# Optimization experiments

Hardware: AMD Instinct MI355X
Metric: run time of the kernel (lower is better)

## Reference

```python
import jax, jax.numpy as jnp
import numpy as np
from jax import lax

B, S, M, D, NQ = 128, 100, 50, 128, 10000


def _xavier(key, shape):
    fan_in, fan_out = shape[0], shape[-1]
    limit = float(np.sqrt(6.0 / (fan_in + fan_out)))
    return jax.random.uniform(key, shape, jnp.float32, -limit, limit)


def setup_inputs() -> dict:
    key = jax.random.key(0)
    ks = jax.random.split(key, 16)
    return {
        "question_seq": jax.random.randint(ks[0], (B, S), 0, NQ),
        "answer_seq": jax.random.randint(ks[1], (B, S), 0, 2),
        "emb": _xavier(ks[2], (NQ, D)),
        "key_matrix": _xavier(ks[3], (M, D)),
        "vu_w1": _xavier(ks[4], (2 * D, D)),
        "vu_b1": jnp.zeros((D,), jnp.float32),
        "vu_w2": _xavier(ks[5], (D, D)),
        "vu_b2": jnp.zeros((D,), jnp.float32),
        "er_w": _xavier(ks[6], (D, D)),
        "er_b": jnp.zeros((D,), jnp.float32),
        "ad_w": _xavier(ks[7], (D, D)),
        "ad_b": jnp.zeros((D,), jnp.float32),
        "out_w1": _xavier(ks[8], (2 * D, D)),
        "out_b1": jnp.zeros((D,), jnp.float32),
        "out_w2": _xavier(ks[9], (D, 1)),
        "out_b2": jnp.zeros((1,), jnp.float32),
    }


def reference(question_seq, answer_seq, emb, key_matrix,
              vu_w1, vu_b1, vu_w2, vu_b2,
              er_w, er_b, ad_w, ad_b,
              out_w1, out_b1, out_w2, out_b2):
    # q_embed for all steps: [B,S,D]; attention over memory slots: [B,S,M]
    q_emb = emb[question_seq]
    attn = jax.nn.softmax(jnp.einsum('bsd,md->bsm', q_emb, key_matrix), axis=-1)

    def step(v, inp):
        w, qe = inp                                   # w: [B,M], qe: [B,D]
        read = jnp.einsum('bm,bmd->bd', w, v)         # attention read
        u = jnp.concatenate([read, qe], axis=-1)      # [B,2D]
        h = jnp.tanh(u @ vu_w1 + vu_b1)
        up = h @ vu_w2 + vu_b2                        # update vector [B,D]
        e = jax.nn.sigmoid(up @ er_w + er_b)          # erase gate
        a = jnp.tanh(up @ ad_w + ad_b)                # add vector
        v = v * (1.0 - w[:, :, None] * e[:, None, :]) + w[:, :, None] * a[:, None, :]
        return v, None

    v0 = jnp.zeros((B, M, D), q_emb.dtype)
    vT, _ = lax.scan(step, v0, (attn.transpose(1, 0, 2), q_emb.transpose(1, 0, 2)))

    # predict with last question (target_question=None branch)
    last_qe = q_emb[:, -1]                            # [B,D]
    last_w = attn[:, -1]                              # [B,M]
    read = jnp.einsum('bm,bmd->bd', last_w, vT)
    p_in = jnp.concatenate([read, last_qe], axis=-1)
    h = jax.nn.relu(p_in @ out_w1 + out_b1)
    pred = jax.nn.sigmoid(h @ out_w2 + out_b2)[:, 0]  # [B]
    return pred
```

## Files before the change

kernel.cpp:

```cpp
#include <hip/hip_runtime.h>

#define BB 128
#define SS 100
#define MM 50
#define DD 128
#define KROW 66

typedef float f32x2 __attribute__((ext_vector_type(2)));

#if defined(__has_builtin)
#  if __has_builtin(__builtin_elementwise_fma)
#    define HAVE_PKFMA 1
#  endif
#  if __has_builtin(__builtin_amdgcn_update_dpp)
#    define HAVE_DPP 1
#  endif
#  if __has_builtin(__builtin_amdgcn_rcpf)
#    define HAVE_RCP 1
#  endif
#endif

__device__ __forceinline__ f32x2 pkfma(f32x2 a, f32x2 b, f32x2 c) {
#ifdef HAVE_PKFMA
    return __builtin_elementwise_fma(a, b, c);
#else
    f32x2 r; r.x = fmaf(a.x, b.x, c.x); r.y = fmaf(a.y, b.y, c.y); return r;
#endif
}

__device__ __forceinline__ float qbf_add(float x) {
#ifdef HAVE_DPP
    union { float f; int i; } c, o;
    c.f = x;
    o.i = __builtin_amdgcn_update_dpp(0, c.i, 0xB1, 0xF, 0xF, true);
    x += o.f;
    c.f = x;
    o.i = __builtin_amdgcn_update_dpp(0, c.i, 0x4E, 0xF, 0xF, true);
    return x + o.f;
#else
    x += __shfl_xor(x, 1);
    x += __shfl_xor(x, 2);
    return x;
#endif
}

__device__ __forceinline__ void barrier_lgkm() {
    asm volatile("s_waitcnt lgkmcnt(0)" ::: "memory");
    __builtin_amdgcn_s_barrier();
    __builtin_amdgcn_sched_barrier(0);
}

__device__ __forceinline__ float bf2f(unsigned short u) {
    union { unsigned int i; float f; } c; c.i = ((unsigned int)u) << 16; return c.f;
}
__device__ __forceinline__ float bfu_lo(unsigned int u) {
    union { unsigned int i; float f; } c; c.i = u << 16; return c.f;
}
__device__ __forceinline__ float bfu_hi(unsigned int u) {
    union { unsigned int i; float f; } c; c.i = u & 0xffff0000u; return c.f;
}
__device__ __forceinline__ unsigned short f2bf_bits(float f) {
    union { float f; unsigned int u; } c; c.f = f;
    unsigned int r = (c.u + 0x7FFFu + ((c.u >> 16) & 1u)) >> 16;
    return (unsigned short)r;
}
__device__ __forceinline__ unsigned int packbf(float lo, float hi) {
    return (unsigned int)f2bf_bits(lo) | ((unsigned int)f2bf_bits(hi) << 16);
}
__device__ __forceinline__ float fast_rcp(float x) {
#ifdef HAVE_RCP
    return __builtin_amdgcn_rcpf(x);
#else
    return 1.0f / x;
#endif
}
__device__ __forceinline__ float fast_sigmoid(float x) {
    return fast_rcp(1.0f + __expf(-x));
}
__device__ __forceinline__ float fast_tanh(float x) {
    float ax = fabsf(x);
    float z = __expf(-2.0f * ax);
    float r = (1.0f - z) * fast_rcp(1.0f + z);
    return copysignf(r, x);
}

template <bool BF16>
__device__ __forceinline__ float ldw(const void* p, size_t idx) {
    if (BF16) return bf2f(((const unsigned short*)p)[idx]);
    return ((const float*)p)[idx];
}

__device__ __forceinline__ bool detect_bf16(const void* emb) {
    const unsigned int* eu = (const unsigned int*)emb;
    int cnt = 0;
    for (int i = 0; i < 32; ++i) {
        unsigned int e8 = (eu[i] >> 7) & 0xFFu;
        cnt += (e8 >= 100u && e8 <= 127u) ? 1 : 0;
    }
    return cnt >= 16;
}

#define W2ROW(r) ((r) * 68 + (((r) >> 5) << 3))

#define WS_WROW_OFF 0u
#define WS_QP_OFF   (BB * SS * 32u * 4u)
#define WS_W2EA_OFF (WS_QP_OFF + BB * SS * DD * 2u)
#define WS_EAB_OFF  (WS_W2EA_OFF + DD * DD * 8u)
#define WS_NEED     (WS_EAB_OFF + DD * 8u)

struct __align__(16) SmemA {
    union {
        struct {
            unsigned int key_w[MM * KROW];
            unsigned int qe8[8][68];
        } pre;
        unsigned int w2s[8724];
    } u;
};

template <bool BF16>
__device__ void pre_impl(const int* qseq, const void* emb, const void* key,
                         const void* vu_w1, unsigned int* wrow_g, unsigned short* qp_g,
                         SmemA& sm)
{
    const int t = threadIdx.x;
    const int b = blockIdx.x;
    const int half = blockIdx.y;
    const int l = t & 63;
    const int wv = t >> 6;
    const int q = l & 3;
    const int d = (wv << 4) + (l >> 2);

    if (BF16) {
        const unsigned int* kg = (const unsigned int*)key;
        for (int g = t; g < MM * 64; g += 512)
            sm.u.pre.key_w[(g >> 6) * KROW + (g & 63)] = kg[g];
    } else {
        const float* kf = (const float*)key;
        for (int g = t; g < MM * 64; g += 512) {
            int row = g >> 6, c2 = g & 63;
            sm.u.pre.key_w[row * KROW + c2] = packbf(kf[row * 128 + 2 * c2], kf[row * 128 + 2 * c2 + 1]);
        }
    }

    float rw1b[32];
#pragma unroll
    for (int i = 0; i < 32; ++i)
        rw1b[i] = ldw<BF16>(vu_w1, (size_t)(DD + 32 * q + i) * DD + d);
    __syncthreads();

    for (int ii = 0; ii < 7; ++ii) {
        const int nrows = (ii == 6) ? 2 : 8;
        {
            int r = t >> 6, w = t & 63;
            if (r < nrows) {
                int s = 50 * half + 8 * ii + r;
                int row = qseq[b * SS + s];
                if (BF16) {
                    sm.u.pre.qe8[r][w] = ((const unsigned int*)emb)[((size_t)row << 6) + w];
                } else {
                    const float* ef = (const float*)emb + (((size_t)row) << 7) + 2 * w;
                    sm.u.pre.qe8[r][w] = packbf(ef[0], ef[1]);
                }
            }
        }
        __syncthreads();

        if (wv < nrows) {
            int m = l;
            int mc = (m < MM) ? m : (MM - 1);
            float a0 = 0.f, a1 = 0.f, a2 = 0.f, a3 = 0.f;
#pragma unroll
            for (int j = 0; j < 32; ++j) {
                uint2 kw = *(const uint2*)&sm.u.pre.key_w[mc * KROW + 2 * j];
                uint2 qw = *(const uint2*)&sm.u.pre.qe8[wv][2 * j];
                a0 = fmaf(bfu_lo(kw.x), bfu_lo(qw.x), a0);
                a1 = fmaf(bfu_hi(kw.x), bfu_hi(qw.x), a1);
                a2 = fmaf(bfu_lo(kw.y), bfu_lo(qw.y), a2);
                a3 = fmaf(bfu_hi(kw.y), bfu_hi(qw.y), a3);
            }
            float lg = (a0 + a1) + (a2 + a3);
            if (m >= MM) lg = -1e30f;
            float mx = lg;
#pragma unroll
            for (int o = 32; o > 0; o >>= 1) mx = fmaxf(mx, __shfl_xor(mx, o));
            float p = (m < MM) ? __expf(lg - mx) : 0.f;
            float sum = p;
#pragma unroll
            for (int o = 32; o > 0; o >>= 1) sum += __shfl_xor(sum, o);
            p = p * fast_rcp(sum);
            float pn = __shfl_xor(p, 4);
            int s = 50 * half + 8 * ii + wv;
            if ((m & 4) == 0)
                wrow_g[(size_t)(b * SS + s) * 32 + (m & 3) * 8 + (m >> 3)] = packbf(p, pn);
        }

        for (int sr = 0; sr < nrows; ++sr) {
            float p0 = 0.f, p1 = 0.f;
#pragma unroll
            for (int i = 0; i < 16; ++i) {
                unsigned int uw = sm.u.pre.qe8[sr][16 * q + i];
                p0 = fmaf(rw1b[2 * i],     bfu_lo(uw), p0);
                p1 = fmaf(rw1b[2 * i + 1], bfu_hi(uw), p1);
            }
            float qpv = qbf_add(p0 + p1);
            int s = 50 * half + 8 * ii + sr;
            if (q == 0) qp_g[(size_t)(b * SS + s) * DD + d] = f2bf_bits(qpv);
        }
        __syncthreads();
    }
}

template <bool BF16>
__device__ void build_impl(const void* vu_w2, const void* vu_b2,
                           const void* er_w, const void* er_b,
                           const void* ad_w, const void* ad_b,
                           f32x2* w2ea_g, f32x2* eab_g, SmemA& sm)
{
    const int t = threadIdx.x;
    const int l = t & 63;
    const int wv = t >> 6;
    const int q = l & 3;
    const int d = (wv << 4) + (l >> 2);

    if (BF16) {
        const unsigned int* wg = (const unsigned int*)vu_w2;
        for (int g = t; g < 128 * 64; g += 512)
            sm.u.w2s[W2ROW(g >> 6) + (g & 63)] = wg[g];
    } else {
        const float* wf = (const float*)vu_w2;
        for (int g = t; g < 128 * 64; g += 512) {
            int row = g >> 6, c2 = g & 63;
            sm.u.w2s[W2ROW(row) + c2] = packbf(wf[row * 128 + 2 * c2], wf[row * 128 + 2 * c2 + 1]);
        }
    }
    __syncthreads();

    f32x2 rw2ea[32];
#pragma unroll
    for (int k = 0; k < 32; ++k) { rw2ea[k].x = 0.f; rw2ea[k].y = 0.f; }
    f32x2 eab2; eab2.x = 0.f; eab2.y = 0.f;
#pragma unroll 1
    for (int jc = 0; jc < 4; ++jc) {
        f32x2 ea[32];
#pragma unroll
        for (int i = 0; i < 32; ++i) {
            int j = 32 * jc + i;
            ea[i].x = ldw<BF16>(er_w, (size_t)j * DD + d);
            ea[i].y = ldw<BF16>(ad_w, (size_t)j * DD + d);
            float b2j = ldw<BF16>(vu_b2, j);
            f32x2 bs; bs.x = b2j; bs.y = b2j;
            eab2 = pkfma(bs, ea[i], eab2);
        }
#pragma unroll
        for (int k = 0; k < 32; ++k) {
            const uint4* wp = (const uint4*)&sm.u.w2s[W2ROW(32 * q + k) + 16 * jc];
            uint4 A = wp[0], B = wp[1], C = wp[2], Dv = wp[3];
            unsigned int W[16] = { A.x, A.y, A.z, A.w, B.x, B.y, B.z, B.w,
                                   C.x, C.y, C.z, C.w, Dv.x, Dv.y, Dv.z, Dv.w };
            f32x2 acc = rw2ea[k];
#pragma unroll
            for (int wd = 0; wd < 16; ++wd) {
                float wlo = bfu_lo(W[wd]), whi = bfu_hi(W[wd]);
                f32x2 s0; s0.x = wlo; s0.y = wlo;
                f32x2 s1; s1.x = whi; s1.y = whi;
                acc = pkfma(s0, ea[2 * wd], acc);
                acc = pkfma(s1, ea[2 * wd + 1], acc);
            }
            rw2ea[k] = acc;
        }
    }
    eab2.x += ldw<BF16>(er_b, d);
    eab2.y += ldw<BF16>(ad_b, d);

#pragma unroll
    for (int k = 0; k < 32; ++k)
        w2ea_g[(size_t)(32 * q + k) * DD + d] = rw2ea[k];
    if (q == 0) eab_g[d] = eab2;
}

__global__ __launch_bounds__(512) void DKVMN_78546361909953_pre(
    const int* __restrict__ qseq,
    const void* emb, const void* key, const void* vu_w1,
    const void* vu_w2, const void* vu_b2,
    const void* er_w, const void* er_b, const void* ad_w, const void* ad_b,
    void* ws)
{
    __shared__ SmemA sm;
    unsigned int*   wrow_g = (unsigned int*)((char*)ws + WS_WROW_OFF);
    unsigned short* qp_g   = (unsigned short*)((char*)ws + WS_QP_OFF);
    f32x2*          w2ea_g = (f32x2*)((char*)ws + WS_W2EA_OFF);
    f32x2*          eab_g  = (f32x2*)((char*)ws + WS_EAB_OFF);
    bool isbf = detect_bf16(emb);
    if (blockIdx.x < BB) {
        if (isbf) pre_impl<true>(qseq, emb, key, vu_w1, wrow_g, qp_g, sm);
        else      pre_impl<false>(qseq, emb, key, vu_w1, wrow_g, qp_g, sm);
    } else if (blockIdx.y == 0) {
        if (isbf) build_impl<true>(vu_w2, vu_b2, er_w, er_b, ad_w, ad_b, w2ea_g, eab_g, sm);
        else      build_impl<false>(vu_w2, vu_b2, er_w, er_b, ad_w, ad_b, w2ea_g, eab_g, sm);
    }
}

struct __align__(16) SmemB {
    float xread[152];
    float xh[152];
    float h1f[DD];
    float qlast[DD];
    unsigned int   wtab[SS][32];
    unsigned short qptab[SS][DD];
};

template <bool BF16>
__device__ void scan_impl(
    const int* __restrict__ qseq,
    const void* emb, const void* vu_w1, const void* vu_b1,
    const void* out_w1, const void* out_b1, const void* out_w2, const void* out_b2,
    const unsigned int* wrow_g, const unsigned short* qp_g,
    const f32x2* w2ea_g, const f32x2* eab_g,
    void* outp, SmemB& sm)
{
    const int t = threadIdx.x;
    const int b = blockIdx.x;
    const int l = t & 63;
    const int q = l & 3;
    const int d = ((t >> 6) << 4) + (l >> 2);

    {
        const uint4* srcw = (const uint4*)(wrow_g + (size_t)b * SS * 32);
        uint4* dstw = (uint4*)&sm.wtab[0][0];
        for (int g = t; g < SS * 32 / 4; g += 512) dstw[g] = srcw[g];
        const uint4* srcq = (const uint4*)(qp_g + (size_t)b * SS * DD);
        uint4* dstq = (uint4*)&sm.qptab[0][0];
        for (int g = t; g < SS * DD / 8; g += 512) dstq[g] = srcq[g];
    }

    if (t < 64) {
        int row = qseq[b * SS + (SS - 1)];
        if (BF16) {
            unsigned int uw = ((const unsigned int*)emb)[((size_t)row << 6) + t];
            sm.qlast[2 * t]     = bfu_lo(uw);
            sm.qlast[2 * t + 1] = bfu_hi(uw);
        } else {
            const float* ef = (const float*)emb + (((size_t)row) << 7) + 2 * t;
            sm.qlast[2 * t]     = ef[0];
            sm.qlast[2 * t + 1] = ef[1];
        }
    }

    f32x2 rw1a2[16];
#pragma unroll
    for (int i = 0; i < 16; ++i) {
        int k0 = 32 * q + 2 * i;
        rw1a2[i].x = ldw<BF16>(vu_w1, (size_t)k0 * DD + d);
        rw1a2[i].y = ldw<BF16>(vu_w1, (size_t)(k0 + 1) * DD + d);
    }
    const float b1r = ldw<BF16>(vu_b1, d);

    f32x2 rwe2[16], rwa2[16];
#pragma unroll
    for (int i = 0; i < 16; ++i) {
        f32x2 w0 = w2ea_g[(size_t)(32 * q + 2 * i) * DD + d];
        f32x2 w1 = w2ea_g[(size_t)(32 * q + 2 * i + 1) * DD + d];
        rwe2[i].x = w0.x; rwe2[i].y = w1.x;
        rwa2[i].x = w0.y; rwa2[i].y = w1.y;
    }
    const f32x2 eab2 = eab_g[d];

    f32x2 v2[7];
#pragma unroll
    for (int p = 0; p < 7; ++p) { v2[p].x = 0.f; v2[p].y = 0.f; }

    if (t < 152) sm.xread[t] = 0.f;
    __syncthreads();

    f32x2 wr2[7];
    {
        uint4 w0 = *(const uint4*)&sm.wtab[0][q * 8];
        uint4 w1 = *(const uint4*)&sm.wtab[0][q * 8 + 4];
        unsigned int ww[8] = { w0.x, w0.y, w0.z, w0.w, w1.x, w1.y, w1.z, w1.w };
#pragma unroll
        for (int p = 0; p < 7; ++p) { wr2[p].x = bfu_lo(ww[p]); wr2[p].y = bfu_hi(ww[p]); }
    }
    unsigned short qpcur = sm.qptab[0][d];

    for (int s = 0; s < SS; ++s) {
        uint4 pwA, pwB;
        unsigned short pq = 0;
        const bool hasnext = (s + 1 < SS);
        if (hasnext) {
            pwA = *(const uint4*)&sm.wtab[s + 1][q * 8];
            pwB = *(const uint4*)&sm.wtab[s + 1][q * 8 + 4];
            pq  = sm.qptab[s + 1][d];
        }

        {
            float hb = bf2f(qpcur) + b1r;
            const float4* xp = (const float4*)&sm.xread[40 * q];
            f32x2 acc0, acc1, acc2, acc3;
            acc0.x = 0.f; acc0.y = 0.f; acc1.x = 0.f; acc1.y = 0.f;
            acc2.x = 0.f; acc2.y = 0.f; acc3.x = 0.f; acc3.y = 0.f;
#pragma unroll
            for (int j = 0; j < 4; ++j) {
                float4 X = xp[2 * j];
                float4 Y = xp[2 * j + 1];
                f32x2 x01; x01.x = X.x; x01.y = X.y;
                f32x2 x23; x23.x = X.z; x23.y = X.w;
                f32x2 y01; y01.x = Y.x; y01.y = Y.y;
                f32x2 y23; y23.x = Y.z; y23.y = Y.w;
                acc0 = pkfma(rw1a2[4 * j],     x01, acc0);
                acc1 = pkfma(rw1a2[4 * j + 1], x23, acc1);
                acc2 = pkfma(rw1a2[4 * j + 2], y01, acc2);
                acc3 = pkfma(rw1a2[4 * j + 3], y23, acc3);
            }
            f32x2 ap = (acc0 + acc1) + (acc2 + acc3);
            float acc = qbf_add(ap.x + ap.y);
            float hh = fast_tanh(acc + hb);
            if (q == 0) sm.xh[d + 8 * (d >> 5)] = hh;
        }
        barrier_lgkm();

        {
            const float4* xp = (const float4*)&sm.xh[40 * q];
            f32x2 ae0, ae1, ae2, ae3, aa0, aa1, aa2, aa3;
            ae0.x = 0.f; ae0.y = 0.f; ae1.x = 0.f; ae1.y = 0.f;
            ae2.x = 0.f; ae2.y = 0.f; ae3.x = 0.f; ae3.y = 0.f;
            aa0.x = 0.f; aa0.y = 0.f; aa1.x = 0.f; aa1.y = 0.f;
            aa2.x = 0.f; aa2.y = 0.f; aa3.x = 0.f; aa3.y = 0.f;
#pragma unroll
            for (int j = 0; j < 4; ++j) {
                float4 X = xp[2 * j];
                float4 Y = xp[2 * j + 1];
                f32x2 h01; h01.x = X.x; h01.y = X.y;
                f32x2 h23; h23.x = X.z; h23.y = X.w;
                f32x2 h45; h45.x = Y.x; h45.y = Y.y;
                f32x2 h67; h67.x = Y.z; h67.y = Y.w;
                ae0 = pkfma(rwe2[4 * j],     h01, ae0);
                aa0 = pkfma(rwa2[4 * j],     h01, aa0);
                ae1 = pkfma(rwe2[4 * j + 1], h23, ae1);
                aa1 = pkfma(rwa2[4 * j + 1], h23, aa1);
                ae2 = pkfma(rwe2[4 * j + 2], h45, ae2);
                aa2 = pkfma(rwa2[4 * j + 2], h45, aa2);
                ae3 = pkfma(rwe2[4 * j + 3], h67, ae3);
                aa3 = pkfma(rwa2[4 * j + 3], h67, aa3);
            }
            f32x2 aep = (ae0 + ae1) + (ae2 + ae3);
            f32x2 aap = (aa0 + aa1) + (aa2 + aa3);
            float ae = qbf_add(aep.x + aep.y);
            float aa = qbf_add(aap.x + aap.y);
            float e = fast_sigmoid(ae + eab2.x);
            float a = fast_tanh(aa + eab2.y);
            f32x2 me; me.x = -e; me.y = -e;
            f32x2 av; av.x = a;  av.y = a;
#pragma unroll
            for (int p = 0; p < 7; ++p)
                v2[p] = pkfma(wr2[p], pkfma(me, v2[p], av), v2[p]);
            if (hasnext) {
                unsigned int ww[8] = { pwA.x, pwA.y, pwA.z, pwA.w, pwB.x, pwB.y, pwB.z, pwB.w };
#pragma unroll
                for (int p = 0; p < 7; ++p) { wr2[p].x = bfu_lo(ww[p]); wr2[p].y = bfu_hi(ww[p]); }
                qpcur = pq;
            }
            f32x2 rA; rA.x = 0.f; rA.y = 0.f;
            f32x2 rB; rB.x = 0.f; rB.y = 0.f;
            rA = pkfma(wr2[0], v2[0], rA); rB = pkfma(wr2[1], v2[1], rB);
            rA = pkfma(wr2[2], v2[2], rA); rB = pkfma(wr2[3], v2[3], rB);
            rA = pkfma(wr2[4], v2[4], rA); rB = pkfma(wr2[5], v2[5], rB);
            rA = pkfma(wr2[6], v2[6], rA);
            float rr = qbf_add((rA.x + rB.x) + (rA.y + rB.y));
            if (q == 0) sm.xread[rr == rr ? (d + 8 * (d >> 5)) : 0] = rr;
        }
        barrier_lgkm();
    }

    float acc = 0.f;
    {
        const float4* xp = (const float4*)&sm.xread[40 * q];
        const float4* qp4 = (const float4*)&sm.qlast[32 * q];
#pragma unroll
        for (int j = 0; j < 8; ++j) {
            float4 xv = xp[j];
            float4 qv = qp4[j];
            int k = 32 * q + 4 * j;
            acc = fmaf(ldw<BF16>(out_w1, (size_t)k * DD + d),       xv.x, acc);
            acc = fmaf(ldw<BF16>(out_w1, (size_t)(k + 1) * DD + d), xv.y, acc);
            acc = fmaf(ldw<BF16>(out_w1, (size_t)(k + 2) * DD + d), xv.z, acc);
            acc = fmaf(ldw<BF16>(out_w1, (size_t)(k + 3) * DD + d), xv.w, acc);
            acc = fmaf(ldw<BF16>(out_w1, (size_t)(DD + k) * DD + d),     qv.x, acc);
            acc = fmaf(ldw<BF16>(out_w1, (size_t)(DD + k + 1) * DD + d), qv.y, acc);
            acc = fmaf(ldw<BF16>(out_w1, (size_t)(DD + k + 2) * DD + d), qv.z, acc);
            acc = fmaf(ldw<BF16>(out_w1, (size_t)(DD + k + 3) * DD + d), qv.w, acc);
        }
    }
    acc = qbf_add(acc);
    float h1 = fmaxf(acc + ldw<BF16>(out_b1, d), 0.f);
    if (q == 0) sm.h1f[d] = h1;
    __syncthreads();

    if (t < 64) {
        float xs = fmaf(sm.h1f[t], ldw<BF16>(out_w2, t),
                        sm.h1f[64 + t] * ldw<BF16>(out_w2, 64 + t));
#pragma unroll
        for (int o = 32; o > 0; o >>= 1) xs += __shfl_xor(xs, o);
        if (t == 0) {
            float pred = fast_sigmoid(xs + ldw<BF16>(out_b2, 0));
            if (BF16) ((unsigned short*)outp)[b] = f2bf_bits(pred);
            else      ((float*)outp)[b] = pred;
        }
    }
}

__global__ __launch_bounds__(512) void DKVMN_78546361909953_scan(
    const int* __restrict__ qseq,
    const void* emb, const void* vu_w1, const void* vu_b1,
    const void* out_w1, const void* out_b1, const void* out_w2, const void* out_b2,
    void* ws, void* outp)
{
    __shared__ SmemB sm;
    const unsigned int*   wrow_g = (const unsigned int*)((char*)ws + WS_WROW_OFF);
    const unsigned short* qp_g   = (const unsigned short*)((char*)ws + WS_QP_OFF);
    const f32x2*          w2ea_g = (const f32x2*)((char*)ws + WS_W2EA_OFF);
    const f32x2*          eab_g  = (const f32x2*)((char*)ws + WS_EAB_OFF);
    if (detect_bf16(emb))
        scan_impl<true>(qseq, emb, vu_w1, vu_b1, out_w1, out_b1, out_w2, out_b2,
                        wrow_g, qp_g, w2ea_g, eab_g, outp, sm);
    else
        scan_impl<false>(qseq, emb, vu_w1, vu_b1, out_w1, out_b1, out_w2, out_b2,
                         wrow_g, qp_g, w2ea_g, eab_g, outp, sm);
}

struct __align__(16) SmemM {
    union {
        struct {
            unsigned int key_w[MM * KROW];
            unsigned int qe8[8][68];
        } pre;
        struct {
            float xread[152];
            float xhdup[312];
            float h1f[DD];
        } run;
    } u;
    union {
        unsigned int w2s[8724];
        struct {
            unsigned int wrow_p[SS][32];
            unsigned short qp_all[SS][DD];
        } tab;
    } v2;
    int qrow[SS];
    float qlast[DD];
};

template <bool BF16>
__device__ void mono_impl(
    const int* __restrict__ qseq,
    const void* emb, const void* key,
    const void* vu_w1, const void* vu_b1, const void* vu_w2, const void* vu_b2,
    const void* er_w, const void* er_b, const void* ad_w, const void* ad_b,
    const void* out_w1, const void* out_b1, const void* out_w2, const void* out_b2,
    void* outp, SmemM& sm)
{
    const int t = threadIdx.x;
    const int b = blockIdx.x;
    const int l = t & 63;
    const int wv = t >> 6;
    const int q = l & 3;
    const int d = (wv << 4) + (l >> 2);

    if (BF16) {
        const unsigned int* kg = (const unsigned int*)key;
        for (int g = t; g < MM * 64; g += 512)
            sm.u.pre.key_w[(g >> 6) * KROW + (g & 63)] = kg[g];
        const unsigned int* wg = (const unsigned int*)vu_w2;
        for (int g = t; g < 128 * 64; g += 512)
            sm.v2.w2s[W2ROW(g >> 6) + (g & 63)] = wg[g];
    } else {
        const float* kf = (const float*)key;
        for (int g = t; g < MM * 64; g += 512) {
            int row = g >> 6, c2 = g & 63;
            sm.u.pre.key_w[row * KROW + c2] = packbf(kf[row * 128 + 2 * c2], kf[row * 128 + 2 * c2 + 1]);
        }
        const float* wf = (const float*)vu_w2;
        for (int g = t; g < 128 * 64; g += 512) {
            int row = g >> 6, c2 = g & 63;
            sm.v2.w2s[W2ROW(row) + c2] = packbf(wf[row * 128 + 2 * c2], wf[row * 128 + 2 * c2 + 1]);
        }
    }
    for (int g = t; g < SS; g += 512) sm.qrow[g] = qseq[b * SS + g];
    __syncthreads();

    f32x2 rw2ea[32];
#pragma unroll
    for (int k = 0; k < 32; ++k) { rw2ea[k].x = 0.f; rw2ea[k].y = 0.f; }
    f32x2 eab2; eab2.x = 0.f; eab2.y = 0.f;
#pragma unroll 1
    for (int jc = 0; jc < 4; ++jc) {
        f32x2 ea[32];
#pragma unroll
        for (int i = 0; i < 32; ++i) {
            int j = 32 * jc + i;
            ea[i].x = ldw<BF16>(er_w, (size_t)j * DD + d);
            ea[i].y = ldw<BF16>(ad_w, (size_t)j * DD + d);
            float b2j = ldw<BF16>(vu_b2, j);
            f32x2 bs; bs.x = b2j; bs.y = b2j;
            eab2 = pkfma(bs, ea[i], eab2);
        }
#pragma unroll
        for (int k = 0; k < 32; ++k) {
            const uint4* wp = (const uint4*)&sm.v2.w2s[W2ROW(32 * q + k) + 16 * jc];
            uint4 A = wp[0], B = wp[1], C = wp[2], Dv = wp[3];
            unsigned int W[16] = { A.x, A.y, A.z, A.w, B.x, B.y, B.z, B.w,
                                   C.x, C.y, C.z, C.w, Dv.x, Dv.y, Dv.z, Dv.w };
            f32x2 acc = rw2ea[k];
#pragma unroll
            for (int wd = 0; wd < 16; ++wd) {
                float wlo = bfu_lo(W[wd]), whi = bfu_hi(W[wd]);
                f32x2 s0; s0.x = wlo; s0.y = wlo;
                f32x2 s1; s1.x = whi; s1.y = whi;
                acc = pkfma(s0, ea[2 * wd], acc);
                acc = pkfma(s1, ea[2 * wd + 1], acc);
            }
            rw2ea[k] = acc;
        }
    }
    eab2.x += ldw<BF16>(er_b, d);
    eab2.y += ldw<BF16>(ad_b, d);
    __syncthreads();

    float rw1a[32], rw1b[32];
#pragma unroll
    for (int i = 0; i < 32; ++i) {
        rw1a[i] = ldw<BF16>(vu_w1, (size_t)(32 * q + i) * DD + d);
        rw1b[i] = ldw<BF16>(vu_w1, (size_t)(DD + 32 * q + i) * DD + d);
    }
    const float b1r = ldw<BF16>(vu_b1, d);

    for (int ii = 0; ii < 13; ++ii) {
        const int nrows = (ii == 12) ? 4 : 8;
        {
            int r = t >> 6, w = t & 63;
            if (r < nrows) {
                int row = sm.qrow[8 * ii + r];
                if (BF16) {
                    sm.u.pre.qe8[r][w] = ((const unsigned int*)emb)[((size_t)row << 6) + w];
                } else {
                    const float* ef = (const float*)emb + (((size_t)row) << 7) + 2 * w;
                    sm.u.pre.qe8[r][w] = packbf(ef[0], ef[1]);
                }
            }
        }
        __syncthreads();

        if (wv < nrows) {
            int m = l;
            int mc = (m < MM) ? m : (MM - 1);
            float a0 = 0.f, a1 = 0.f, a2 = 0.f, a3 = 0.f;
#pragma unroll
            for (int j = 0; j < 32; ++j) {
                uint2 kw = *(const uint2*)&sm.u.pre.key_w[mc * KROW + 2 * j];
                uint2 qw = *(const uint2*)&sm.u.pre.qe8[wv][2 * j];
                a0 = fmaf(bfu_lo(kw.x), bfu_lo(qw.x), a0);
                a1 = fmaf(bfu_hi(kw.x), bfu_hi(qw.x), a1);
                a2 = fmaf(bfu_lo(kw.y), bfu_lo(qw.y), a2);
                a3 = fmaf(bfu_hi(kw.y), bfu_hi(qw.y), a3);
            }
            float lg = (a0 + a1) + (a2 + a3);
            if (m >= MM) lg = -1e30f;
            float mx = lg;
#pragma unroll
            for (int o = 32; o > 0; o >>= 1) mx = fmaxf(mx, __shfl_xor(mx, o));
            float p = (m < MM) ? __expf(lg - mx) : 0.f;
            float sum = p;
#pragma unroll
            for (int o = 32; o > 0; o >>= 1) sum += __shfl_xor(sum, o);
            p = p * fast_rcp(sum);
            float pn = __shfl_xor(p, 4);
            if ((m & 4) == 0)
                sm.v2.tab.wrow_p[8 * ii + wv][(m & 3) * 8 + (m >> 3)] = packbf(p, pn);
        }

        for (int sr = 0; sr < nrows; ++sr) {
            float p0 = 0.f, p1 = 0.f;
#pragma unroll
            for (int i = 0; i < 16; ++i) {
                unsigned int uw = sm.u.pre.qe8[sr][16 * q + i];
                p0 = fmaf(rw1b[2 * i],     bfu_lo(uw), p0);
                p1 = fmaf(rw1b[2 * i + 1], bfu_hi(uw), p1);
            }
            float qpv = qbf_add(p0 + p1);
            if (q == 0) sm.v2.tab.qp_all[8 * ii + sr][d] = f2bf_bits(qpv);
        }
        __syncthreads();
    }

    if (t < 64) {
        unsigned int uw = sm.u.pre.qe8[3][t];
        sm.qlast[2 * t]     = bfu_lo(uw);
        sm.qlast[2 * t + 1] = bfu_hi(uw);
    }
    f32x2 v2[7];
#pragma unroll
    for (int p = 0; p < 7; ++p) { v2[p].x = 0.f; v2[p].y = 0.f; }
    f32x2 wr2[7];
    {
        const uint4* wp = (const uint4*)&sm.v2.tab.wrow_p[0][q * 8];
        uint4 w0 = wp[0], w1 = wp[1];
        unsigned int ww[8] = { w0.x, w0.y, w0.z, w0.w, w1.x, w1.y, w1.z, w1.w };
#pragma unroll
        for (int p = 0; p < 7; ++p) { wr2[p].x = bfu_lo(ww[p]); wr2[p].y = bfu_hi(ww[p]); }
    }
    if (t < 152) sm.u.run.xread[t] = 0.f;
    __syncthreads();

    for (int s = 0; s < SS; ++s) {
        {
            float qpv = bf2f(sm.v2.tab.qp_all[s][d]);
            const float4* xp = (const float4*)&sm.u.run.xread[40 * q];
            f32x2 rw1a2_j;
            f32x2 acc2; acc2.x = 0.f; acc2.y = 0.f;
#pragma unroll
            for (int j = 0; j < 8; ++j) {
                float4 X = xp[j];
                f32x2 x01; x01.x = X.x; x01.y = X.y;
                f32x2 x23; x23.x = X.z; x23.y = X.w;
                rw1a2_j.x = rw1a[4 * j];     rw1a2_j.y = rw1a[4 * j + 1];
                acc2 = pkfma(rw1a2_j, x01, acc2);
                rw1a2_j.x = rw1a[4 * j + 2]; rw1a2_j.y = rw1a[4 * j + 3];
                acc2 = pkfma(rw1a2_j, x23, acc2);
            }
            float acc = qbf_add(acc2.x + acc2.y);
            float hh = fast_tanh(acc + qpv + b1r);
            if (q == 0) {
                f32x2 hd; hd.x = hh; hd.y = hh;
                *(f32x2*)&sm.u.run.xhdup[2 * d + 8 * ((2 * d) >> 5)] = hd;
            }
        }
        __syncthreads();

        {
            f32x2 acc2; acc2.x = 0.f; acc2.y = 0.f;
#pragma unroll
            for (int blk = 0; blk < 2; ++blk) {
                const float4* xp = (const float4*)&sm.u.run.xhdup[80 * q + 40 * blk];
#pragma unroll
                for (int j = 0; j < 8; ++j) {
                    float4 X = xp[j];
                    f32x2 s0; s0.x = X.x; s0.y = X.y;
                    f32x2 s1; s1.x = X.z; s1.y = X.w;
                    int k = 16 * blk + 2 * j;
                    acc2 = pkfma(rw2ea[k], s0, acc2);
                    acc2 = pkfma(rw2ea[k + 1], s1, acc2);
                }
            }
            float ae = qbf_add(acc2.x);
            float aa = qbf_add(acc2.y);
            float e = fast_sigmoid(ae + eab2.x);
            float a = fast_tanh(aa + eab2.y);
            f32x2 me; me.x = -e; me.y = -e;
            f32x2 av; av.x = a;  av.y = a;
#pragma unroll
            for (int p = 0; p < 7; ++p)
                v2[p] = pkfma(wr2[p], pkfma(me, v2[p], av), v2[p]);
            if (s + 1 < SS) {
                const uint4* wp = (const uint4*)&sm.v2.tab.wrow_p[s + 1][q * 8];
                uint4 w0 = wp[0], w1 = wp[1];
                unsigned int ww[8] = { w0.x, w0.y, w0.z, w0.w, w1.x, w1.y, w1.z, w1.w };
#pragma unroll
                for (int p = 0; p < 7; ++p) { wr2[p].x = bfu_lo(ww[p]); wr2[p].y = bfu_hi(ww[p]); }
            }
            f32x2 racc; racc.x = 0.f; racc.y = 0.f;
#pragma unroll
            for (int p = 0; p < 7; ++p)
                racc = pkfma(wr2[p], v2[p], racc);
            float rr = qbf_add(racc.x + racc.y);
            if (q == 0) sm.u.run.xread[d + 8 * (d >> 5)] = rr;
        }
        __syncthreads();
    }

    float acc = 0.f;
    {
        const float4* xp = (const float4*)&sm.u.run.xread[40 * q];
        const float4* qp4 = (const float4*)&sm.qlast[32 * q];
#pragma unroll
        for (int j = 0; j < 8; ++j) {
            float4 xv = xp[j];
            float4 qv = qp4[j];
            int k = 32 * q + 4 * j;
            acc = fmaf(ldw<BF16>(out_w1, (size_t)k * DD + d),       xv.x, acc);
            acc = fmaf(ldw<BF16>(out_w1, (size_t)(k + 1) * DD + d), xv.y, acc);
            acc = fmaf(ldw<BF16>(out_w1, (size_t)(k + 2) * DD + d), xv.z, acc);
            acc = fmaf(ldw<BF16>(out_w1, (size_t)(k + 3) * DD + d), xv.w, acc);
            acc = fmaf(ldw<BF16>(out_w1, (size_t)(DD + k) * DD + d),     qv.x, acc);
            acc = fmaf(ldw<BF16>(out_w1, (size_t)(DD + k + 1) * DD + d), qv.y, acc);
            acc = fmaf(ldw<BF16>(out_w1, (size_t)(DD + k + 2) * DD + d), qv.z, acc);
            acc = fmaf(ldw<BF16>(out_w1, (size_t)(DD + k + 3) * DD + d), qv.w, acc);
        }
    }
    acc = qbf_add(acc);
    float h1 = fmaxf(acc + ldw<BF16>(out_b1, d), 0.f);
    if (q == 0) sm.u.run.h1f[d] = h1;
    __syncthreads();

    if (t < 64) {
        float xs = fmaf(sm.u.run.h1f[t], ldw<BF16>(out_w2, t),
                        sm.u.run.h1f[64 + t] * ldw<BF16>(out_w2, 64 + t));
#pragma unroll
        for (int o = 32; o > 0; o >>= 1) xs += __shfl_xor(xs, o);
        if (t == 0) {
            float pred = fast_sigmoid(xs + ldw<BF16>(out_b2, 0));
            if (BF16) ((unsigned short*)outp)[b] = f2bf_bits(pred);
            else      ((float*)outp)[b] = pred;
        }
    }
}

__global__ __launch_bounds__(512) void DKVMN_78546361909953_kernel(
    const int* __restrict__ qseq,
    const void* emb, const void* key,
    const void* vu_w1, const void* vu_b1, const void* vu_w2, const void* vu_b2,
    const void* er_w, const void* er_b, const void* ad_w, const void* ad_b,
    const void* out_w1, const void* out_b1, const void* out_w2, const void* out_b2,
    void* outp)
{
    __shared__ SmemM sm;
    if (detect_bf16(emb))
        mono_impl<true>(qseq, emb, key, vu_w1, vu_b1, vu_w2, vu_b2,
                        er_w, er_b, ad_w, ad_b, out_w1, out_b1, out_w2, out_b2, outp, sm);
    else
        mono_impl<false>(qseq, emb, key, vu_w1, vu_b1, vu_w2, vu_b2,
                         er_w, er_b, ad_w, ad_b, out_w1, out_b1, out_w2, out_b2, outp, sm);
}

extern "C" void kernel_launch(void* const* d_in, const int* in_sizes, int n_in,
                              void* d_out, int out_size, void* d_ws, size_t ws_size,
                              hipStream_t stream) {
    const int* qseq = (const int*)d_in[0];
    if (ws_size >= (size_t)WS_NEED) {
        DKVMN_78546361909953_pre<<<dim3(BB + 1, 2), 512, 0, stream>>>(
            qseq, d_in[2], d_in[3], d_in[4],
            d_in[6], d_in[7], d_in[8], d_in[9], d_in[10], d_in[11], d_ws);
        DKVMN_78546361909953_scan<<<BB, 512, 0, stream>>>(
            qseq, d_in[2], d_in[4], d_in[5],
            d_in[12], d_in[13], d_in[14], d_in[15], d_ws, d_out);
    } else {
        DKVMN_78546361909953_kernel<<<BB, 512, 0, stream>>>(
            qseq, d_in[2], d_in[3], d_in[4], d_in[5], d_in[6], d_in[7],
            d_in[8], d_in[9], d_in[10], d_in[11],
            d_in[12], d_in[13], d_in[14], d_in[15], d_out);
    }
}
```

Baseline: 247.0 us.

## Use bf16 dot2 instructions and bf16 shared vectors in scan recurrence

Rewrites the per-step scan to store the read and hidden vectors in shared memory as bf16 and compute the matvecs with v_dot2_f32_bf16 on packed bf16 weight registers. Memory weights are pre-expanded to fp32 in shared memory, the loop is unrolled by two with ping-pong weight registers, exp is replaced by exp2 intrinsics, and launch bounds request two blocks per CU. The aim is to shorten the serial per-step critical path and cut register pressure, at the cost of extra bf16 rounding on intermediate activations and weights.

```diff
diff --git a/kernel.cpp b/kernel.cpp
--- a/kernel.cpp
+++ b/kernel.cpp
@@ -18,6 +18,15 @@
 #  if __has_builtin(__builtin_amdgcn_rcpf)
 #    define HAVE_RCP 1
 #  endif
+#  if __has_builtin(__builtin_amdgcn_exp2f)
+#    define EXP2(x) __builtin_amdgcn_exp2f(x)
+#  endif
+#  if __has_builtin(__builtin_amdgcn_fdot2_f32_bf16)
+#    define HAVE_DOT2BF 1
+#  endif
+#endif
+#ifndef EXP2
+#  define EXP2(x) exp2f(x)
 #endif
 
 __device__ __forceinline__ f32x2 pkfma(f32x2 a, f32x2 b, f32x2 c) {
@@ -67,6 +76,13 @@
 __device__ __forceinline__ unsigned int packbf(float lo, float hi) {
     return (unsigned int)f2bf_bits(lo) | ((unsigned int)f2bf_bits(hi) << 16);
 }
+__device__ __forceinline__ unsigned short f2bf_hw(float f) {
+#ifdef HAVE_DOT2BF
+    union { __bf16 b; unsigned short u; } c; c.b = (__bf16)f; return c.u;
+#else
+    return f2bf_bits(f);
+#endif
+}
 __device__ __forceinline__ float fast_rcp(float x) {
 #ifdef HAVE_RCP
     return __builtin_amdgcn_rcpf(x);
@@ -75,14 +91,24 @@
 #endif
 }
 __device__ __forceinline__ float fast_sigmoid(float x) {
-    return fast_rcp(1.0f + __expf(-x));
+    return fast_rcp(1.0f + EXP2(x * -1.4426950408889634f));
 }
 __device__ __forceinline__ float fast_tanh(float x) {
     float ax = fabsf(x);
-    float z = __expf(-2.0f * ax);
+    float z = EXP2(ax * -2.8853900817779268f);
     float r = (1.0f - z) * fast_rcp(1.0f + z);
     return copysignf(r, x);
 }
+
+#ifdef HAVE_DOT2BF
+typedef __bf16 bf2v __attribute__((ext_vector_type(2)));
+__device__ __forceinline__ bf2v u2bf(unsigned int u) {
+    union { unsigned int x; bf2v v; } c; c.x = u; return c.v;
+}
+__device__ __forceinline__ float dot2bf(unsigned int a, unsigned int b, float c) {
+    return __builtin_amdgcn_fdot2_f32_bf16(u2bf(a), u2bf(b), c, false);
+}
+#endif
 
 template <bool BF16>
 __device__ __forceinline__ float ldw(const void* p, size_t idx) {
@@ -302,13 +328,141 @@
 }
 
 struct __align__(16) SmemB {
-    float xread[152];
-    float xh[152];
+    unsigned short xread[144];
+    unsigned short xh[144];
     float h1f[DD];
     float qlast[DD];
-    unsigned int   wtab[SS][32];
+    f32x2 wtabf[SS][32];
     unsigned short qptab[SS][DD];
 };
+
+#ifdef HAVE_DOT2BF
+#define SCAN_E(HB)                                                          \
+    {                                                                       \
+        const uint4* xp_ = (const uint4*)&sm.xread[32 * q];                 \
+        uint4 X0 = xp_[0], X1 = xp_[1], X2 = xp_[2], X3 = xp_[3];           \
+        float a0_ = dot2bf(rw1p[0],  X0.x, (HB) * 0.25f);                   \
+        float a1_ = dot2bf(rw1p[1],  X0.y, 0.f);                            \
+        float a2_ = dot2bf(rw1p[2],  X0.z, 0.f);                            \
+        float a3_ = dot2bf(rw1p[3],  X0.w, 0.f);                            \
+        a0_ = dot2bf(rw1p[4],  X1.x, a0_);                                  \
+        a1_ = dot2bf(rw1p[5],  X1.y, a1_);                                  \
+        a2_ = dot2bf(rw1p[6],  X1.z, a2_);                                  \
+        a3_ = dot2bf(rw1p[7],  X1.w, a3_);                                  \
+        a0_ = dot2bf(rw1p[8],  X2.x, a0_);                                  \
+        a1_ = dot2bf(rw1p[9],  X2.y, a1_);                                  \
+        a2_ = dot2bf(rw1p[10], X2.z, a2_);                                  \
+        a3_ = dot2bf(rw1p[11], X2.w, a3_);                                  \
+        a0_ = dot2bf(rw1p[12], X3.x, a0_);                                  \
+        a1_ = dot2bf(rw1p[13], X3.y, a1_);                                  \
+        a2_ = dot2bf(rw1p[14], X3.z, a2_);                                  \
+        a3_ = dot2bf(rw1p[15], X3.w, a3_);                                  \
+        float u_ = qbf_add((a0_ + a1_) + (a2_ + a3_));                      \
+        float hh_ = fast_tanh(u_);                                          \
+        if (q == 0) sm.xh[d] = f2bf_hw(hh_);                                \
+    }
+#define SCAN_G_ACC                                                          \
+        const uint4* hp_ = (const uint4*)&sm.xh[32 * q];                    \
+        uint4 H0 = hp_[0], H1 = hp_[1], H2 = hp_[2], H3 = hp_[3];           \
+        float e0_ = dot2bf(rwep[0],  H0.x, eab2.x * 0.25f);                 \
+        float g0_ = dot2bf(rwap[0],  H0.x, eab2.y * 0.25f);                 \
+        float e1_ = dot2bf(rwep[1],  H0.y, 0.f);                            \
+        float g1_ = dot2bf(rwap[1],  H0.y, 0.f);                            \
+        float e2_ = dot2bf(rwep[2],  H0.z, 0.f);                            \
+        float g2_ = dot2bf(rwap[2],  H0.z, 0.f);                            \
+        float e3_ = dot2bf(rwep[3],  H0.w, 0.f);                            \
+        float g3_ = dot2bf(rwap[3],  H0.w, 0.f);                            \
+        e0_ = dot2bf(rwep[4],  H1.x, e0_);  g0_ = dot2bf(rwap[4],  H1.x, g0_); \
+        e1_ = dot2bf(rwep[5],  H1.y, e1_);  g1_ = dot2bf(rwap[5],  H1.y, g1_); \
+        e2_ = dot2bf(rwep[6],  H1.z, e2_);  g2_ = dot2bf(rwap[6],  H1.z, g2_); \
+        e3_ = dot2bf(rwep[7],  H1.w, e3_);  g3_ = dot2bf(rwap[7],  H1.w, g3_); \
+        e0_ = dot2bf(rwep[8],  H2.x, e0_);  g0_ = dot2bf(rwap[8],  H2.x, g0_); \
+        e1_ = dot2bf(rwep[9],  H2.y, e1_);  g1_ = dot2bf(rwap[9],  H2.y, g1_); \
+        e2_ = dot2bf(rwep[10], H2.z, e2_);  g2_ = dot2bf(rwap[10], H2.z, g2_); \
+        e3_ = dot2bf(rwep[11], H2.w, e3_);  g3_ = dot2bf(rwap[11], H2.w, g3_); \
+        e0_ = dot2bf(rwep[12], H3.x, e0_);  g0_ = dot2bf(rwap[12], H3.x, g0_); \
+        e1_ = dot2bf(rwep[13], H3.y, e1_);  g1_ = dot2bf(rwap[13], H3.y, g1_); \
+        e2_ = dot2bf(rwep[14], H3.z, e2_);  g2_ = dot2bf(rwap[14], H3.z, g2_); \
+        e3_ = dot2bf(rwep[15], H3.w, e3_);  g3_ = dot2bf(rwap[15], H3.w, g3_); \
+        float ae_ = qbf_add((e0_ + e1_) + (e2_ + e3_));                     \
+        float aa_ = qbf_add((g0_ + g1_) + (g2_ + g3_));
+#else
+#define SCAN_E(HB)                                                          \
+    {                                                                       \
+        const uint4* xp_ = (const uint4*)&sm.xread[32 * q];                 \
+        uint4 X0 = xp_[0], X1 = xp_[1], X2 = xp_[2], X3 = xp_[3];           \
+        unsigned int XW_[16] = { X0.x, X0.y, X0.z, X0.w, X1.x, X1.y, X1.z, X1.w, \
+                                 X2.x, X2.y, X2.z, X2.w, X3.x, X3.y, X3.z, X3.w }; \
+        float a0_ = (HB) * 0.25f, a1_ = 0.f, a2_ = 0.f, a3_ = 0.f;          \
+        _Pragma("unroll")                                                   \
+        for (int i_ = 0; i_ < 4; ++i_) {                                    \
+            a0_ = fmaf(rw1a[8 * i_ + 0], bfu_lo(XW_[4 * i_ + 0]), a0_);     \
+            a0_ = fmaf(rw1a[8 * i_ + 1], bfu_hi(XW_[4 * i_ + 0]), a0_);     \
+            a1_ = fmaf(rw1a[8 * i_ + 2], bfu_lo(XW_[4 * i_ + 1]), a1_);     \
+            a1_ = fmaf(rw1a[8 * i_ + 3], bfu_hi(XW_[4 * i_ + 1]), a1_);     \
+            a2_ = fmaf(rw1a[8 * i_ + 4], bfu_lo(XW_[4 * i_ + 2]), a2_);     \
+            a2_ = fmaf(rw1a[8 * i_ + 5], bfu_hi(XW_[4 * i_ + 2]), a2_);     \
+            a3_ = fmaf(rw1a[8 * i_ + 6], bfu_lo(XW_[4 * i_ + 3]), a3_);     \
+            a3_ = fmaf(rw1a[8 * i_ + 7], bfu_hi(XW_[4 * i_ + 3]), a3_);     \
+        }                                                                   \
+        float u_ = qbf_add((a0_ + a1_) + (a2_ + a3_));                      \
+        float hh_ = fast_tanh(u_);                                          \
+        if (q == 0) sm.xh[d] = f2bf_hw(hh_);                                \
+    }
+#define SCAN_G_ACC                                                          \
+        const uint4* hp_ = (const uint4*)&sm.xh[32 * q];                    \
+        uint4 H0 = hp_[0], H1 = hp_[1], H2 = hp_[2], H3 = hp_[3];           \
+        unsigned int HW_[16] = { H0.x, H0.y, H0.z, H0.w, H1.x, H1.y, H1.z, H1.w, \
+                                 H2.x, H2.y, H2.z, H2.w, H3.x, H3.y, H3.z, H3.w }; \
+        float ae_ = eab2.x * 0.25f, aa_ = eab2.y * 0.25f;                   \
+        float e1_ = 0.f, g1_ = 0.f;                                         \
+        _Pragma("unroll")                                                   \
+        for (int i_ = 0; i_ < 16; ++i_) {                                   \
+            float lo_ = bfu_lo(HW_[i_]), hi_ = bfu_hi(HW_[i_]);             \
+            ae_ = fmaf(rwe[2 * i_], lo_, ae_);                              \
+            e1_ = fmaf(rwe[2 * i_ + 1], hi_, e1_);                          \
+            aa_ = fmaf(rwa[2 * i_], lo_, aa_);                              \
+            g1_ = fmaf(rwa[2 * i_ + 1], hi_, g1_);                          \
+        }                                                                   \
+        ae_ = qbf_add(ae_ + e1_);                                           \
+        aa_ = qbf_add(aa_ + g1_);
+#endif
+
+#define SCAN_STEP(S, WR, WN, LAST)                                          \
+    {                                                                       \
+        float hb_ = bf2f(qpcur) + b1r;                                      \
+        if (!(LAST)) {                                                      \
+            const float4* wp4_ = (const float4*)&sm.wtabf[(S) + 1][q * 8];  \
+            float4 Aw = wp4_[0], Bw = wp4_[1], Cw = wp4_[2], Dw = wp4_[3];  \
+            WN[0] = Aw.x;  WN[1] = Aw.y;  WN[2] = Aw.z;  WN[3] = Aw.w;      \
+            WN[4] = Bw.x;  WN[5] = Bw.y;  WN[6] = Bw.z;  WN[7] = Bw.w;      \
+            WN[8] = Cw.x;  WN[9] = Cw.y;  WN[10] = Cw.z; WN[11] = Cw.w;     \
+            WN[12] = Dw.x; WN[13] = Dw.y;                                   \
+            pq = sm.qptab[(S) + 1][d];                                      \
+        }                                                                   \
+        SCAN_E(hb_)                                                         \
+        barrier_lgkm();                                                     \
+        {                                                                   \
+            SCAN_G_ACC                                                      \
+            float e_ = fast_sigmoid(ae_);                                   \
+            float a_ = fast_tanh(aa_);                                      \
+            _Pragma("unroll")                                               \
+            for (int m_ = 0; m_ < 14; ++m_)                                 \
+                vv[m_] = fmaf(WR[m_], fmaf(-e_, vv[m_], a_), vv[m_]);       \
+            const float* wu_ = (LAST) ? WR : WN;                            \
+            float r0_ = wu_[0] * vv[0], r1_ = wu_[1] * vv[1];               \
+            float r2_ = wu_[2] * vv[2], r3_ = wu_[3] * vv[3];               \
+            r0_ = fmaf(wu_[4],  vv[4],  r0_); r1_ = fmaf(wu_[5],  vv[5],  r1_); \
+            r2_ = fmaf(wu_[6],  vv[6],  r2_); r3_ = fmaf(wu_[7],  vv[7],  r3_); \
+            r0_ = fmaf(wu_[8],  vv[8],  r0_); r1_ = fmaf(wu_[9],  vv[9],  r1_); \
+            r2_ = fmaf(wu_[10], vv[10], r2_); r3_ = fmaf(wu_[11], vv[11], r3_); \
+            r0_ = fmaf(wu_[12], vv[12], r0_); r1_ = fmaf(wu_[13], vv[13], r1_); \
+            float rr_ = qbf_add((r0_ + r1_) + (r2_ + r3_));                 \
+            if (q == 0) sm.xread[d] = f2bf_hw(rr_);                         \
+            if (!(LAST)) qpcur = pq;                                        \
+        }                                                                   \
+        barrier_lgkm();                                                     \
+    }
 
 template <bool BF16>
 __device__ void scan_impl(
@@ -326,9 +480,13 @@
     const int d = ((t >> 6) << 4) + (l >> 2);
 
     {
-        const uint4* srcw = (const uint4*)(wrow_g + (size_t)b * SS * 32);
-        uint4* dstw = (uint4*)&sm.wtab[0][0];
-        for (int g = t; g < SS * 32 / 4; g += 512) dstw[g] = srcw[g];
+        const unsigned int* srcw = wrow_g + (size_t)b * SS * 32;
+        f32x2* dstw = (f32x2*)&sm.wtabf[0][0];
+        for (int g = t; g < SS * 32; g += 512) {
+            unsigned int u = srcw[g];
+            f32x2 v; v.x = bfu_lo(u); v.y = bfu_hi(u);
+            dstw[g] = v;
+        }
         const uint4* srcq = (const uint4*)(qp_g + (size_t)b * SS * DD);
         uint4* dstq = (uint4*)&sm.qptab[0][0];
         for (int g = t; g < SS * DD / 8; g += 512) dstq[g] = srcq[g];
@@ -347,144 +505,74 @@
         }
     }
 
-    f32x2 rw1a2[16];
+    const float b1r = ldw<BF16>(vu_b1, d);
+    const f32x2 eab2 = eab_g[d];
+
+#ifdef HAVE_DOT2BF
+    unsigned int rw1p[16], rwep[16], rwap[16];
 #pragma unroll
     for (int i = 0; i < 16; ++i) {
         int k0 = 32 * q + 2 * i;
-        rw1a2[i].x = ldw<BF16>(vu_w1, (size_t)k0 * DD + d);
-        rw1a2[i].y = ldw<BF16>(vu_w1, (size_t)(k0 + 1) * DD + d);
-    }
-    const float b1r = ldw<BF16>(vu_b1, d);
-
-    f32x2 rwe2[16], rwa2[16];
-#pragma unroll
-    for (int i = 0; i < 16; ++i) {
-        f32x2 w0 = w2ea_g[(size_t)(32 * q + 2 * i) * DD + d];
-        f32x2 w1 = w2ea_g[(size_t)(32 * q + 2 * i + 1) * DD + d];
-        rwe2[i].x = w0.x; rwe2[i].y = w1.x;
-        rwa2[i].x = w0.y; rwa2[i].y = w1.y;
-    }
-    const f32x2 eab2 = eab_g[d];
-
-    f32x2 v2[7];
-#pragma unroll
-    for (int p = 0; p < 7; ++p) { v2[p].x = 0.f; v2[p].y = 0.f; }
-
-    if (t < 152) sm.xread[t] = 0.f;
+        rw1p[i] = packbf(ldw<BF16>(vu_w1, (size_t)k0 * DD + d),
+                         ldw<BF16>(vu_w1, (size_t)(k0 + 1) * DD + d));
+        f32x2 w0v = w2ea_g[(size_t)k0 * DD + d];
+        f32x2 w1v = w2ea_g[(size_t)(k0 + 1) * DD + d];
+        rwep[i] = packbf(w0v.x, w1v.x);
+        rwap[i] = packbf(w0v.y, w1v.y);
+    }
+#else
+    float rw1a[32], rwe[32], rwa[32];
+#pragma unroll
+    for (int i = 0; i < 32; ++i) {
+        rw1a[i] = ldw<BF16>(vu_w1, (size_t)(32 * q + i) * DD + d);
+        f32x2 wv = w2ea_g[(size_t)(32 * q + i) * DD + d];
+        rwe[i] = wv.x; rwa[i] = wv.y;
+    }
+#endif
+
+    float vv[14];
+#pragma unroll
+    for (int m = 0; m < 14; ++m) vv[m] = 0.f;
+
+    if (t < 144) sm.xread[t] = 0;
     __syncthreads();
 
-    f32x2 wr2[7];
+    float w0[14], w1[14];
     {
-        uint4 w0 = *(const uint4*)&sm.wtab[0][q * 8];
-        uint4 w1 = *(const uint4*)&sm.wtab[0][q * 8 + 4];
-        unsigned int ww[8] = { w0.x, w0.y, w0.z, w0.w, w1.x, w1.y, w1.z, w1.w };
-#pragma unroll
-        for (int p = 0; p < 7; ++p) { wr2[p].x = bfu_lo(ww[p]); wr2[p].y = bfu_hi(ww[p]); }
+        const float4* wp4 = (const float4*)&sm.wtabf[0][q * 8];
+        float4 Aw = wp4[0], Bw = wp4[1], Cw = wp4[2], Dw = wp4[3];
+        w0[0] = Aw.x;  w0[1] = Aw.y;  w0[2] = Aw.z;  w0[3] = Aw.w;
+        w0[4] = Bw.x;  w0[5] = Bw.y;  w0[6] = Bw.z;  w0[7] = Bw.w;
+        w0[8] = Cw.x;  w0[9] = Cw.y;  w0[10] = Cw.z; w0[11] = Cw.w;
+        w0[12] = Dw.x; w0[13] = Dw.y;
     }
     unsigned short qpcur = sm.qptab[0][d];
-
-    for (int s = 0; s < SS; ++s) {
-        uint4 pwA, pwB;
-        unsigned short pq = 0;
-        const bool hasnext = (s + 1 < SS);
-        if (hasnext) {
-            pwA = *(const uint4*)&sm.wtab[s + 1][q * 8];
-            pwB = *(const uint4*)&sm.wtab[s + 1][q * 8 + 4];
-            pq  = sm.qptab[s + 1][d];
-        }
-
-        {
-            float hb = bf2f(qpcur) + b1r;
-            const float4* xp = (const float4*)&sm.xread[40 * q];
-            f32x2 acc0, acc1, acc2, acc3;
-            acc0.x = 0.f; acc0.y = 0.f; acc1.x = 0.f; acc1.y = 0.f;
-            acc2.x = 0.f; acc2.y = 0.f; acc3.x = 0.f; acc3.y = 0.f;
-#pragma unroll
-            for (int j = 0; j < 4; ++j) {
-                float4 X = xp[2 * j];
-                float4 Y = xp[2 * j + 1];
-                f32x2 x01; x01.x = X.x; x01.y = X.y;
-                f32x2 x23; x23.x = X.z; x23.y = X.w;
-                f32x2 y01; y01.x = Y.x; y01.y = Y.y;
-                f32x2 y23; y23.x = Y.z; y23.y = Y.w;
-                acc0 = pkfma(rw1a2[4 * j],     x01, acc0);
-                acc1 = pkfma(rw1a2[4 * j + 1], x23, acc1);
-                acc2 = pkfma(rw1a2[4 * j + 2], y01, acc2);
-                acc3 = pkfma(rw1a2[4 * j + 3], y23, acc3);
-            }
-            f32x2 ap = (acc0 + acc1) + (acc2 + acc3);
-            float acc = qbf_add(ap.x + ap.y);
-            float hh = fast_tanh(acc + hb);
-            if (q == 0) sm.xh[d + 8 * (d >> 5)] = hh;
-        }
-        barrier_lgkm();
-
-        {
-            const float4* xp = (const float4*)&sm.xh[40 * q];
-            f32x2 ae0, ae1, ae2, ae3, aa0, aa1, aa2, aa3;
-            ae0.x = 0.f; ae0.y = 0.f; ae1.x = 0.f; ae1.y = 0.f;
-            ae2.x = 0.f; ae2.y = 0.f; ae3.x = 0.f; ae3.y = 0.f;
-            aa0.x = 0.f; aa0.y = 0.f; aa1.x = 0.f; aa1.y = 0.f;
-            aa2.x = 0.f; aa2.y = 0.f; aa3.x = 0.f; aa3.y = 0.f;
-#pragma unroll
-            for (int j = 0; j < 4; ++j) {
-                float4 X = xp[2 * j];
-                float4 Y = xp[2 * j + 1];
-                f32x2 h01; h01.x = X.x; h01.y = X.y;
-                f32x2 h23; h23.x = X.z; h23.y = X.w;
-                f32x2 h45; h45.x = Y.x; h45.y = Y.y;
-                f32x2 h67; h67.x = Y.z; h67.y = Y.w;
-                ae0 = pkfma(rwe2[4 * j],     h01, ae0);
-                aa0 = pkfma(rwa2[4 * j],     h01, aa0);
-                ae1 = pkfma(rwe2[4 * j + 1], h23, ae1);
-                aa1 = pkfma(rwa2[4 * j + 1], h23, aa1);
-                ae2 = pkfma(rwe2[4 * j + 2], h45, ae2);
-                aa2 = pkfma(rwa2[4 * j + 2], h45, aa2);
-                ae3 = pkfma(rwe2[4 * j + 3], h67, ae3);
-                aa3 = pkfma(rwa2[4 * j + 3], h67, aa3);
-            }
-            f32x2 aep = (ae0 + ae1) + (ae2 + ae3);
-            f32x2 aap = (aa0 + aa1) + (aa2 + aa3);
-            float ae = qbf_add(aep.x + aep.y);
-            float aa = qbf_add(aap.x + aap.y);
-            float e = fast_sigmoid(ae + eab2.x);
-            float a = fast_tanh(aa + eab2.y);
-            f32x2 me; me.x = -e; me.y = -e;
-            f32x2 av; av.x = a;  av.y = a;
-#pragma unroll
-            for (int p = 0; p < 7; ++p)
-                v2[p] = pkfma(wr2[p], pkfma(me, v2[p], av), v2[p]);
-            if (hasnext) {
-                unsigned int ww[8] = { pwA.x, pwA.y, pwA.z, pwA.w, pwB.x, pwB.y, pwB.z, pwB.w };
-#pragma unroll
-                for (int p = 0; p < 7; ++p) { wr2[p].x = bfu_lo(ww[p]); wr2[p].y = bfu_hi(ww[p]); }
-                qpcur = pq;
-            }
-            f32x2 rA; rA.x = 0.f; rA.y = 0.f;
-            f32x2 rB; rB.x = 0.f; rB.y = 0.f;
-            rA = pkfma(wr2[0], v2[0], rA); rB = pkfma(wr2[1], v2[1], rB);
-            rA = pkfma(wr2[2], v2[2], rA); rB = pkfma(wr2[3], v2[3], rB);
-            rA = pkfma(wr2[4], v2[4], rA); rB = pkfma(wr2[5], v2[5], rB);
-            rA = pkfma(wr2[6], v2[6], rA);
-            float rr = qbf_add((rA.x + rB.x) + (rA.y + rB.y));
-            if (q == 0) sm.xread[rr == rr ? (d + 8 * (d >> 5)) : 0] = rr;
-        }
-        barrier_lgkm();
-    }
+    unsigned short pq = qpcur;
+
+    for (int k = 0; k < 49; ++k) {
+        SCAN_STEP(2 * k,     w0, w1, false)
+        SCAN_STEP(2 * k + 1, w1, w0, false)
+    }
+    SCAN_STEP(98, w0, w1, false)
+    SCAN_STEP(99, w1, w0, true)
 
     float acc = 0.f;
     {
-        const float4* xp = (const float4*)&sm.xread[40 * q];
+        const uint4* xw4 = (const uint4*)&sm.xread[32 * q];
+        uint4 W0 = xw4[0], W1 = xw4[1], W2 = xw4[2], W3 = xw4[3];
+        unsigned int XW[16] = { W0.x, W0.y, W0.z, W0.w, W1.x, W1.y, W1.z, W1.w,
+                                W2.x, W2.y, W2.z, W2.w, W3.x, W3.y, W3.z, W3.w };
+#pragma unroll
+        for (int i = 0; i < 16; ++i) {
+            int k = 32 * q + 2 * i;
+            acc = fmaf(ldw<BF16>(out_w1, (size_t)k * DD + d),       bfu_lo(XW[i]), acc);
+            acc = fmaf(ldw<BF16>(out_w1, (size_t)(k + 1) * DD + d), bfu_hi(XW[i]), acc);
+        }
         const float4* qp4 = (const float4*)&sm.qlast[32 * q];
 #pragma unroll
         for (int j = 0; j < 8; ++j) {
-            float4 xv = xp[j];
             float4 qv = qp4[j];
             int k = 32 * q + 4 * j;
-            acc = fmaf(ldw<BF16>(out_w1, (size_t)k * DD + d),       xv.x, acc);
-            acc = fmaf(ldw<BF16>(out_w1, (size_t)(k + 1) * DD + d), xv.y, acc);
-            acc = fmaf(ldw<BF16>(out_w1, (size_t)(k + 2) * DD + d), xv.z, acc);
-            acc = fmaf(ldw<BF16>(out_w1, (size_t)(k + 3) * DD + d), xv.w, acc);
             acc = fmaf(ldw<BF16>(out_w1, (size_t)(DD + k) * DD + d),     qv.x, acc);
             acc = fmaf(ldw<BF16>(out_w1, (size_t)(DD + k + 1) * DD + d), qv.y, acc);
             acc = fmaf(ldw<BF16>(out_w1, (size_t)(DD + k + 2) * DD + d), qv.z, acc);
@@ -509,7 +597,7 @@
     }
 }
 
-__global__ __launch_bounds__(512) void DKVMN_78546361909953_scan(
+__global__ __launch_bounds__(512, 2) void DKVMN_78546361909953_scan(
     const int* __restrict__ qseq,
     const void* emb, const void* vu_w1, const void* vu_b1,
     const void* out_w1, const void* out_b1, const void* out_w2, const void* out_b2,
```

After: 237.4 us. 1.04x faster.
